# Kernel tuning notes

Hardware: AMD Instinct MI355X
Metric: run time of the kernel (lower is better)

## Reference

```python
import jax, jax.numpy as jnp
import numpy as np

EMB = 128
WIN = 5
OUT = 128
VOCAB = 50257
PAD_IDX = 0


def setup_inputs() -> dict:
    key = jax.random.key(0)
    k1, k2, k3 = jax.random.split(key, 3)
    x = jax.random.randint(k1, (16, 2048), 0, VOCAB, dtype=jnp.int64 if jax.config.jax_enable_x64 else jnp.int32)
    emb_table = jax.random.normal(k2, (VOCAB, EMB), dtype=jnp.float32)
    emb_table = emb_table.at[PAD_IDX].set(0.0)  # padding_idx row is zero
    fan_in = EMB * WIN
    bound = 1.0 / np.sqrt(fan_in)
    kw, kb = jax.random.split(k3)
    W = jax.random.uniform(kw, (OUT, fan_in), minval=-bound, maxval=bound, dtype=jnp.float32)
    b = jax.random.uniform(kb, (OUT,), minval=-bound, maxval=bound, dtype=jnp.float32)
    return {"x": x, "emb_table": emb_table, "W": W, "b": b}


def reference(x, emb_table, W, b):
    B, S = x.shape
    no_pads = (WIN - 1) // 2
    emb = emb_table[x]                                   # (B, S, EMB) gather
    padded = jnp.pad(emb, ((0, 0), (no_pads, no_pads), (0, 0)))
    windows = jnp.stack([padded[:, k:k + S] for k in range(WIN)], axis=2)
    flat = windows.reshape(B, S, WIN * EMB)
    y = jnp.einsum('bsk,ok->bso', flat, W) + b           # (B, S, OUT)
    return jax.nn.gelu(y, approximate=False)             # torch GELU default is exact
```

## Files before the change

### kernel.cpp

```cpp
#include <hip/hip_runtime.h>
#include <hip/hip_bf16.h>


#define EMB   128
#define WIN   5
#define OUTC  128
#define SEQ   2048
#define KTOT  640
#define MTILE 64

#define EMB_STRIDE 136

typedef __bf16  bf16x8 __attribute__((ext_vector_type(8)));
typedef float   f32x4  __attribute__((ext_vector_type(4)));
typedef ushort  u16x8  __attribute__((ext_vector_type(8)));

__device__ inline ushort f2bf(float f) {
    __bf16 h = (__bf16)f;
    return __builtin_bit_cast(ushort, h);
}

__device__ inline u16x8 cvt8v(float4 v0, float4 v1) {
    u16x8 o;
    o[0] = f2bf(v0.x); o[1] = f2bf(v0.y); o[2] = f2bf(v0.z); o[3] = f2bf(v0.w);
    o[4] = f2bf(v1.x); o[5] = f2bf(v1.y); o[6] = f2bf(v1.z); o[7] = f2bf(v1.w);
    return o;
}

__global__ __launch_bounds__(256, 4) void conv_encoder_kernel(
    const int* __restrict__ x,
    const float* __restrict__ emb,
    const float* __restrict__ W,
    const float* __restrict__ bias,
    float* __restrict__ out)
{
    __shared__ ushort sEmb[(MTILE + WIN - 1) * EMB_STRIDE];

    const int tid = threadIdx.x;
    const int m0  = blockIdx.x * MTILE;
    const int bb  = m0 >> 11;
    const int s0  = m0 & (SEQ - 1);

    {
        const int xbase = bb * SEQ;
        for (int idx = tid; idx < (MTILE + WIN - 1) * 16; idx += 256) {
            const int r = idx >> 4, c = idx & 15;
            const int s = s0 - 2 + r;
            const int tok = (s >= 0 && s < SEQ) ? x[xbase + s] : 0;
            const float* p = emb + (size_t)tok * EMB + c * 8;
            *(u16x8*)(&sEmb[r * EMB_STRIDE + c * 8]) =
                cvt8v(*(const float4*)p, *(const float4*)(p + 4));
        }
    }
    __syncthreads();

    const int lane = tid & 63;
    const int wv   = tid >> 6;
    const int lr   = lane & 15;
    const int lk8  = (lane >> 4) * 8;

    f32x4 acc[4][2];
    #pragma unroll
    for (int i = 0; i < 4; ++i)
        #pragma unroll
        for (int j = 0; j < 2; ++j)
            acc[i][j] = (f32x4){0.f, 0.f, 0.f, 0.f};

    const float* w0 = W + (size_t)(wv * 32 + lr) * KTOT + lk8;
    const float* w1 = w0 + 16 * KTOT;

    #pragma unroll
    for (int win = 0; win < WIN; ++win) {
        #pragma unroll
        for (int kc = 0; kc < 4; ++kc) {
            const int e  = kc * 32 + lk8;
            const int ko = win * EMB + kc * 32;
            bf16x8 bfr[2], afr[4];
            bfr[0] = __builtin_bit_cast(bf16x8,
                cvt8v(*(const float4*)(w0 + ko), *(const float4*)(w0 + ko + 4)));
            bfr[1] = __builtin_bit_cast(bf16x8,
                cvt8v(*(const float4*)(w1 + ko), *(const float4*)(w1 + ko + 4)));
            #pragma unroll
            for (int i = 0; i < 4; ++i)
                afr[i] = *(const bf16x8*)(&sEmb[(i * 16 + lr + win) * EMB_STRIDE + e]);
            #pragma unroll
            for (int i = 0; i < 4; ++i)
                #pragma unroll
                for (int j = 0; j < 2; ++j)
                    acc[i][j] = __builtin_amdgcn_mfma_f32_16x16x32_bf16(afr[i], bfr[j], acc[i][j], 0, 0, 0);
        }
    }

    float bj[2];
    #pragma unroll
    for (int j = 0; j < 2; ++j)
        bj[j] = bias[wv * 32 + j * 16 + lr];

    const int rbase = (lane >> 4) * 4;
    #pragma unroll
    for (int i = 0; i < 4; ++i) {
        #pragma unroll
        for (int j = 0; j < 2; ++j) {
            const int col = wv * 32 + j * 16 + lr;
            #pragma unroll
            for (int r = 0; r < 4; ++r) {
                const int row = m0 + i * 16 + rbase + r;
                const float y = acc[i][j][r] + bj[j];
                const float g = 0.5f * y * (1.0f + erff(y * 0.70710678118654752f));
                out[(size_t)row * OUTC + col] = g;
            }
        }
    }
}

extern "C" void kernel_launch(void* const* d_in, const int* in_sizes, int n_in,
                              void* d_out, int out_size, void* d_ws, size_t ws_size,
                              hipStream_t stream) {
    (void)in_sizes; (void)n_in; (void)d_ws; (void)ws_size; (void)out_size;
    const int* x        = (const int*)d_in[0];
    const float* emb    = (const float*)d_in[1];
    const float* Wm     = (const float*)d_in[2];
    const float* bias   = (const float*)d_in[3];
    float* out          = (float*)d_out;

    dim3 grid(32768 / MTILE);
    dim3 block(256);
    hipLaunchKernelGGL(conv_encoder_kernel, grid, block, 0, stream, x, emb, Wm, bias, out);
}
```

Before: 103.2 us.

## Split output channels across grid and batch embedding gather loads

Adds a second grid dimension that splits the 128 output channels into two 64-wide tiles. Each block's four waves now cover a 2x2 arrangement of 32x32 sub-tiles, which doubles block count and cuts per-thread accumulators to raise parallelism and occupancy. The cost is that each block gathers and converts the same embedding rows as its sibling, so gather traffic doubles. The gather loop is also unrolled so all token loads, then all embedding loads, are issued before any conversion, which adds memory-level parallelism.

New measurement: 119.6 us. 15.9% more time.

```diff
diff --git a/kernel.cpp b/kernel.cpp
--- a/kernel.cpp
+++ b/kernel.cpp
@@ -8,8 +8,10 @@
 #define SEQ   2048
 #define KTOT  640
 #define MTILE 64
+#define NTILE 64
 
 #define EMB_STRIDE 136
+#define NCHUNK ((MTILE + WIN - 1) * 16)
 
 typedef __bf16  bf16x8 __attribute__((ext_vector_type(8)));
 typedef float   f32x4  __attribute__((ext_vector_type(4)));
@@ -38,35 +40,56 @@
 
     const int tid = threadIdx.x;
     const int m0  = blockIdx.x * MTILE;
+    const int n0  = blockIdx.y * NTILE;
     const int bb  = m0 >> 11;
     const int s0  = m0 & (SEQ - 1);
 
     {
         const int xbase = bb * SEQ;
-        for (int idx = tid; idx < (MTILE + WIN - 1) * 16; idx += 256) {
-            const int r = idx >> 4, c = idx & 15;
-            const int s = s0 - 2 + r;
-            const int tok = (s >= 0 && s < SEQ) ? x[xbase + s] : 0;
-            const float* p = emb + (size_t)tok * EMB + c * 8;
-            *(u16x8*)(&sEmb[r * EMB_STRIDE + c * 8]) =
-                cvt8v(*(const float4*)p, *(const float4*)(p + 4));
+        int tok[5];
+        #pragma unroll
+        for (int u = 0; u < 5; ++u) {
+            const int idx = tid + u * 256;
+            if (idx < NCHUNK) {
+                const int s = s0 - 2 + (idx >> 4);
+                tok[u] = (s >= 0 && s < SEQ) ? x[xbase + s] : 0;
+            }
+        }
+        float4 v0[5], v1[5];
+        #pragma unroll
+        for (int u = 0; u < 5; ++u) {
+            const int idx = tid + u * 256;
+            if (idx < NCHUNK) {
+                const float* p = emb + (size_t)tok[u] * EMB + (idx & 15) * 8;
+                v0[u] = *(const float4*)p;
+                v1[u] = *(const float4*)(p + 4);
+            }
+        }
+        #pragma unroll
+        for (int u = 0; u < 5; ++u) {
+            const int idx = tid + u * 256;
+            if (idx < NCHUNK)
+                *(u16x8*)(&sEmb[(idx >> 4) * EMB_STRIDE + (idx & 15) * 8]) =
+                    cvt8v(v0[u], v1[u]);
         }
     }
     __syncthreads();
 
     const int lane = tid & 63;
     const int wv   = tid >> 6;
+    const int qr   = (wv >> 1) * 32;
+    const int qc   = (wv & 1) * 32;
     const int lr   = lane & 15;
     const int lk8  = (lane >> 4) * 8;
 
-    f32x4 acc[4][2];
+    f32x4 acc[2][2];
     #pragma unroll
-    for (int i = 0; i < 4; ++i)
+    for (int i = 0; i < 2; ++i)
         #pragma unroll
         for (int j = 0; j < 2; ++j)
             acc[i][j] = (f32x4){0.f, 0.f, 0.f, 0.f};
 
-    const float* w0 = W + (size_t)(wv * 32 + lr) * KTOT + lk8;
+    const float* w0 = W + (size_t)(n0 + qc + lr) * KTOT + lk8;
     const float* w1 = w0 + 16 * KTOT;
 
     #pragma unroll
@@ -75,16 +98,16 @@
         for (int kc = 0; kc < 4; ++kc) {
             const int e  = kc * 32 + lk8;
             const int ko = win * EMB + kc * 32;
-            bf16x8 bfr[2], afr[4];
+            bf16x8 bfr[2], afr[2];
             bfr[0] = __builtin_bit_cast(bf16x8,
                 cvt8v(*(const float4*)(w0 + ko), *(const float4*)(w0 + ko + 4)));
             bfr[1] = __builtin_bit_cast(bf16x8,
                 cvt8v(*(const float4*)(w1 + ko), *(const float4*)(w1 + ko + 4)));
             #pragma unroll
-            for (int i = 0; i < 4; ++i)
-                afr[i] = *(const bf16x8*)(&sEmb[(i * 16 + lr + win) * EMB_STRIDE + e]);
+            for (int i = 0; i < 2; ++i)
+                afr[i] = *(const bf16x8*)(&sEmb[(qr + i * 16 + lr + win) * EMB_STRIDE + e]);
             #pragma unroll
-            for (int i = 0; i < 4; ++i)
+            for (int i = 0; i < 2; ++i)
                 #pragma unroll
                 for (int j = 0; j < 2; ++j)
                     acc[i][j] = __builtin_amdgcn_mfma_f32_16x16x32_bf16(afr[i], bfr[j], acc[i][j], 0, 0, 0);
@@ -94,17 +117,17 @@
     float bj[2];
     #pragma unroll
     for (int j = 0; j < 2; ++j)
-        bj[j] = bias[wv * 32 + j * 16 + lr];
+        bj[j] = bias[n0 + qc + j * 16 + lr];
 
     const int rbase = (lane >> 4) * 4;
     #pragma unroll
-    for (int i = 0; i < 4; ++i) {
+    for (int i = 0; i < 2; ++i) {
         #pragma unroll
         for (int j = 0; j < 2; ++j) {
-            const int col = wv * 32 + j * 16 + lr;
+            const int col = n0 + qc + j * 16 + lr;
             #pragma unroll
             for (int r = 0; r < 4; ++r) {
-                const int row = m0 + i * 16 + rbase + r;
+                const int row = m0 + qr + i * 16 + rbase + r;
                 const float y = acc[i][j][r] + bj[j];
                 const float g = 0.5f * y * (1.0f + erff(y * 0.70710678118654752f));
                 out[(size_t)row * OUTC + col] = g;
@@ -123,7 +146,7 @@
     const float* bias   = (const float*)d_in[3];
     float* out          = (float*)d_out;
 
-    dim3 grid(32768 / MTILE);
+    dim3 grid(32768 / MTILE, OUTC / NTILE);
     dim3 block(256);
     hipLaunchKernelGGL(conv_encoder_kernel, grid, block, 0, stream, x, emb, Wm, bias, out);
 }
```
